# Kernel optimization log

Hardware: AMD Instinct MI355X
Metric: run time of the kernel (lower is better)

## Reference

```python
import jax, jax.numpy as jnp
import numpy as np

CHAN = 24
INNER = 64
GROUPS = 8
M = 5
LAM = 1e-4
MAX_ITER = 25
BETA = 1.0
EPS = 1e-5
B, HH, WW = 128, 32, 32


def conv2d(x, w, b=None):
    # NCHW, OIHW, 3x3 SAME conv (padding = kernel//2)
    y = jax.lax.conv_general_dilated(x, w, (1, 1), 'SAME',
                                     dimension_numbers=('NCHW', 'OIHW', 'NCHW'))
    if b is not None:
        y = y + b[None, :, None, None]
    return y


def group_norm(x, g, b):
    bsz, c, h, w = x.shape
    xg = x.reshape(bsz, GROUPS, c // GROUPS, h, w)
    mu = xg.mean(axis=(2, 3, 4), keepdims=True)
    var = xg.var(axis=(2, 3, 4), keepdims=True)
    xn = ((xg - mu) / jnp.sqrt(var + EPS)).reshape(bsz, c, h, w)
    return xn * g[None, :, None, None] + b[None, :, None, None]


def batch_norm(x, g, b):
    # training-mode batch statistics over (N, H, W)
    mu = x.mean(axis=(0, 2, 3), keepdims=True)
    var = x.var(axis=(0, 2, 3), keepdims=True)
    return (x - mu) / jnp.sqrt(var + EPS) * g[None, :, None, None] + b[None, :, None, None]


def resnet_f(p, z, x):
    c1w, g1g, g1b, c2w, g2g, g2b, g3g, g3b = p
    y = group_norm(jax.nn.relu(conv2d(z, c1w)), g1g, g1b)
    return group_norm(jax.nn.relu(z + group_norm(x + conv2d(y, c2w), g2g, g2b)), g3g, g3b)


def anderson(f, x0):
    # Anderson acceleration, fixed MAX_ITER iterations (no host-sync tol break).
    bsz = x0.shape[0]
    d = x0.size // bsz
    X = jnp.zeros((bsz, M, d), x0.dtype)
    Fm = jnp.zeros((bsz, M, d), x0.dtype)
    f0 = f(x0).reshape(bsz, -1)
    X = X.at[:, 0].set(x0.reshape(bsz, -1))
    Fm = Fm.at[:, 0].set(f0)
    X = X.at[:, 1].set(f0)
    Fm = Fm.at[:, 1].set(f(f0.reshape(x0.shape)).reshape(bsz, -1))
    for k in range(2, MAX_ITER):
        n = min(k, M)
        G = Fm[:, :n] - X[:, :n]                       # [b, n, d]
        Hm = jnp.zeros((bsz, n + 1, n + 1), x0.dtype)
        Hm = Hm.at[:, 0, 1:].set(1.0).at[:, 1:, 0].set(1.0)
        Hm = Hm.at[:, 1:, 1:].set(jnp.einsum('bnd,bmd->bnm', G, G)
                                  + LAM * jnp.eye(n, dtype=x0.dtype)[None])
        yv = jnp.zeros((bsz, n + 1, 1), x0.dtype).at[:, 0, 0].set(1.0)
        alpha = jnp.linalg.solve(Hm, yv)[:, 1:, 0]     # [b, n]
        xnew = (BETA * jnp.einsum('bn,bnd->bd', alpha, Fm[:, :n])
                + (1.0 - BETA) * jnp.einsum('bn,bnd->bd', alpha, X[:, :n]))
        X = X.at[:, k % M].set(xnew)
        Fm = Fm.at[:, k % M].set(f(xnew.reshape(x0.shape)).reshape(bsz, -1))
    return X[:, (MAX_ITER - 1) % M].reshape(x0.shape)


def setup_inputs() -> dict:
    key = jax.random.key(0)
    ks = jax.random.split(key, 8)
    inp = {
        'x': jax.random.normal(ks[0], (B, 3, HH, WW), jnp.float32),
        'pre_conv_w': jax.random.normal(ks[1], (CHAN, 3, 3, 3), jnp.float32) * 0.1,
        'pre_conv_b': jnp.zeros((CHAN,), jnp.float32),
        'pre_bn_g': jnp.ones((CHAN,), jnp.float32),
        'pre_bn_b': jnp.zeros((CHAN,), jnp.float32),
        'f_conv1_w': jax.random.normal(ks[2], (INNER, CHAN, 3, 3), jnp.float32) * 0.01,
        'gn1_g': jnp.ones((INNER,), jnp.float32),
        'gn1_b': jnp.zeros((INNER,), jnp.float32),
        'f_conv2_w': jax.random.normal(ks[3], (CHAN, INNER, 3, 3), jnp.float32) * 0.01,
        'gn2_g': jnp.ones((CHAN,), jnp.float32),
        'gn2_b': jnp.zeros((CHAN,), jnp.float32),
        'gn3_g': jnp.ones((CHAN,), jnp.float32),
        'gn3_b': jnp.zeros((CHAN,), jnp.float32),
        'post_bn_g': jnp.ones((CHAN,), jnp.float32),
        'post_bn_b': jnp.zeros((CHAN,), jnp.float32),
        'fc_w': jax.random.normal(ks[4], (10, CHAN * 4 * 4), jnp.float32) * 0.05,
        'fc_b': jnp.zeros((10,), jnp.float32),
    }
    return inp


def reference(x, pre_conv_w, pre_conv_b, pre_bn_g, pre_bn_b,
              f_conv1_w, gn1_g, gn1_b, f_conv2_w, gn2_g, gn2_b, gn3_g, gn3_b,
              post_bn_g, post_bn_b, fc_w, fc_b):
    # pre: conv + BatchNorm
    xp = batch_norm(conv2d(x, pre_conv_w, pre_conv_b), pre_bn_g, pre_bn_b)
    p = (f_conv1_w, gn1_g, gn1_b, f_conv2_w, gn2_g, gn2_b, gn3_g, gn3_b)
    # DEQ fixed-point solve (eval path: train=False returns the fixed point)
    z_star = anderson(lambda z: resnet_f(p, z, xp), jnp.zeros_like(xp))
    z = resnet_f(p, z_star, xp)
    # post: relu -> BN -> avgpool(8,8) -> flatten -> linear
    h = batch_norm(jax.nn.relu(z), post_bn_g, post_bn_b)
    bsz, c, hh, ww = h.shape
    pooled = h.reshape(bsz, c, hh // 8, 8, ww // 8, 8).mean(axis=(3, 5))  # [B,C,4,4]
    return pooled.reshape(bsz, -1) @ fc_w.T + fc_b
```

## Files before the change

### kernel.cpp

```cpp
#include <hip/hip_runtime.h>
#include <hip/hip_bf16.h>

typedef __hip_bfloat16 bf16;
typedef unsigned short ushortT;
typedef __attribute__((ext_vector_type(8))) short short8;
typedef __attribute__((ext_vector_type(4))) float f32x4;

#define BB 128
#define CHAN 24
#define INNER 64
#define HW 1024
#define DD (CHAN*HW)

constexpr size_t cBD = (size_t)BB*DD;
constexpr size_t cYB = (size_t)BB*INNER*HW;

__device__ __attribute__((aligned(16))) ushortT g_xp[cBD];
__device__ __attribute__((aligned(16))) ushortT g_X[5*cBD];
__device__ __attribute__((aligned(16))) ushortT g_F[5*cBD];
__device__ __attribute__((aligned(16))) ushortT g_G[5*cBD];
__device__ __attribute__((aligned(16))) ushortT g_yb[cYB];
__device__ __attribute__((aligned(16))) ushortT g_tb[cBD];
__device__ __attribute__((aligned(16))) ushortT g_w1m[9*64*32];
__device__ __attribute__((aligned(16))) ushortT g_w2m[9*24*64];
__device__ __attribute__((aligned(16))) float g_stats2a[48];
__device__ __attribute__((aligned(16))) float g_stats2b[48];
__device__ __attribute__((aligned(16))) float g_gn1sum[BB*8*2];
__device__ __attribute__((aligned(16))) float g_gn2sum[BB*24*2];
__device__ __attribute__((aligned(16))) float g_gram[BB*25];
__device__ __attribute__((aligned(16))) float g_params[5120];
__device__ unsigned g_isbf16;

#define P_PCW 0
#define P_PCB 648
#define P_PBG 672
#define P_PBB 696
#define P_G1G 720
#define P_G1B 784
#define P_G2G 848
#define P_G2B 872
#define P_G3G 896
#define P_G3B 920
#define P_POG 944
#define P_POB 968
#define P_FCW 992
#define P_FCB 4832

__device__ __forceinline__ size_t aidx(int b, int icv, int pix){
  return (((size_t)b*3 + icv)*1024 + (size_t)pix)*8;
}
__device__ __forceinline__ float rdin(const void* p, int i){
  if (g_isbf16) return __bfloat162float(((const bf16*)p)[i]);
  return ((const float*)p)[i];
}
__device__ __forceinline__ float b2f(ushortT u){
  unsigned v = ((unsigned)u) << 16;
  return __builtin_bit_cast(float, v);
}
__device__ __forceinline__ ushortT f2b(float f){
  unsigned u = __builtin_bit_cast(unsigned, f);
  u += 0x7FFFu + ((u >> 16) & 1u);
  return (ushortT)(u >> 16);
// ... 17 lines not shown
}

__global__ void detect_k(const void* g1g){
  if (threadIdx.x==0 && blockIdx.x==0){
    unsigned u = *(const unsigned*)g1g;
    g_isbf16 = (u == 0x3F803F80u) ? 1u : 0u;
  }
}

__global__ void cvt_params_k(const void* pcw, const void* pcb, const void* pbg, const void* pbb,
                             const void* g1g, const void* g1b, const void* g2g, const void* g2b,
                             const void* g3g, const void* g3b, const void* pog, const void* pob,
                             const void* fcw, const void* fcb){
  int t = threadIdx.x;
  for (int i=t;i<648;i+=256)  g_params[P_PCW+i]=rdin(pcw,i);
  for (int i=t;i<24;i+=256) { g_params[P_PCB+i]=rdin(pcb,i);
                              g_params[P_PBG+i]=rdin(pbg,i);
                              g_params[P_PBB+i]=rdin(pbb,i);
                              g_params[P_G2G+i]=rdin(g2g,i);
                              g_params[P_G2B+i]=rdin(g2b,i);
                              g_params[P_G3G+i]=rdin(g3g,i);
                              g_params[P_G3B+i]=rdin(g3b,i);
                              g_params[P_POG+i]=rdin(pog,i);
                              g_params[P_POB+i]=rdin(pob,i); }
  for (int i=t;i<64;i+=256) { g_params[P_G1G+i]=rdin(g1g,i);
                              g_params[P_G1B+i]=rdin(g1b,i); }
  for (int i=t;i<3840;i+=256) g_params[P_FCW+i]=rdin(fcw,i);
  for (int i=t;i<10;i+=256)   g_params[P_FCB+i]=rdin(fcb,i);
  for (int i=t;i<48;i+=256) { g_stats2a[i]=0.f; g_stats2b[i]=0.f; }
}

__global__ void wtm_k(const void* w1, const void* w2){
  int t = blockIdx.x*256 + threadIdx.x;
  if (t < 9*64*32){
    int ic = t & 31, oc = (t>>5)&63, s9 = t>>11;
    float v = (ic<24) ? rdin(w1, (oc*24+ic)*9 + s9) : 0.f;
    g_w1m[t] = f2b(v);
  }
  int u = t - 9*64*32;
  if (u >= 0 && u < 9*24*64){
    int ic = u & 63; int rest = u >> 6; int oc = rest % 24; int s9 = rest / 24;
    g_w2m[u] = f2b(rdin(w2, (oc*64+ic)*9 + s9));
  }
}

__global__ void zero0_k(){
  size_t base = ((size_t)blockIdx.x*256 + threadIdx.x)*8;
  short8 z = {0,0,0,0,0,0,0,0};
  *(short8*)&g_yb[base] = z;
  if (blockIdx.x < 1536) *(short8*)&g_X[base] = z;
  int t = blockIdx.x*256 + threadIdx.x;
  if (blockIdx.x < 8)  g_gn1sum[t] = 0.f;
  if (blockIdx.x < 24) g_gn2sum[t] = 0.f;
}

__global__ void preconv_k(const void* __restrict__ x){
  __shared__ float sR2d[4*48];
  int id = blockIdx.x*256 + threadIdx.x;
  int b = id >> 10, pix = id & 1023;
  int yy = pix >> 5, xx = pix & 31;
  float acc[24];
  #pragma unroll
  for (int oc=0;oc<24;oc++) acc[oc] = g_params[P_PCB+oc];
  for (int ic=0; ic<3; ic++)
    for (int ky=0; ky<3; ky++){
      int gy = yy+ky-1; if (gy<0||gy>=32) continue;
      for (int kx=0;kx<3;kx++){
        int gx = xx+kx-1; if (gx<0||gx>=32) continue;
        float v = rdin(x, ((b*3+ic)*32+gy)*32+gx);
        #pragma unroll
        for (int oc=0;oc<24;oc++)
          acc[oc] += v * g_params[P_PCW+(oc*3+ic)*9+ky*3+kx];
      }
    }
  st24c(g_tb, b, pix, acc);
  int lane = threadIdx.x & 63, wv = threadIdx.x >> 6;
  #pragma unroll
  for (int c=0;c<24;c++){
    float r = acc[c], q = acc[c]*acc[c];
    #pragma unroll
    for (int off=32;off;off>>=1){ r += __shfl_down(r,off,64); q += __shfl_down(q,off,64); }
    if (lane==0){ sR2d[wv*48+c*2]=r; sR2d[wv*48+c*2+1]=q; }
  }
  __syncthreads();
  if (threadIdx.x < 48)
    atomicAdd(&g_stats2a[threadIdx.x],
      sR2d[threadIdx.x] + sR2d[48+threadIdx.x] + sR2d[96+threadIdx.x] + sR2d[144+threadIdx.x]);
}

__global__ void bn_apply_k(){
  int id = blockIdx.x*256+threadIdx.x;
  int b = id >> 10, pix = id & 1023;
  const float inv = 1.f/(BB*HW);
  float tv[24], ov[24];
  ld24c(g_tb, b, pix, tv);
  #pragma unroll
  for (int c=0;c<24;c++){
    float mean = g_stats2a[c*2]*inv;
    float var = fmaxf(g_stats2a[c*2+1]*inv - mean*mean, 0.f);
    float rstd = rsqrtf(var + 1e-5f);
    ov[c] = (tv[c]-mean)*rstd*g_params[P_PBG+c] + g_params[P_PBB+c];
  }
  st24c(g_xp, b, pix, ov);
}

__launch_bounds__(256, 2)
__global__ void conv1_k(int s){
  __shared__ ushortT sMem[29312];
  ushortT* sA = sMem;
  ushortT* sW = sMem + 10880;
  const int tid = threadIdx.x;
  const int lane = tid & 63, wv = tid >> 6;
  const int mLane = lane & 15, q = lane >> 4;
  const int b = blockIdx.x >> 2, yt = blockIdx.x & 3;
  const ushortT* __restrict__ Xs = g_X + (size_t)s*cBD;
  if (blockIdx.x < 24) g_gn2sum[blockIdx.x*256 + tid] = 0.f;
  for (int i = tid; i < 1360; i += 256){
    int icv = i & 3, apix = i >> 2;
    int yl = apix / 34, xl = apix - yl*34;
    int gy = yt*8 - 1 + yl, gx = xl - 1;
    short8 v = {0,0,0,0,0,0,0,0};
    if (gy >= 0 && gy < 32 && gx >= 0 && gx < 32 && icv < 3)
      v = *(const short8*)&Xs[aidx(b, icv, gy*32 + gx)];
    *(short8*)&sA[(size_t)(apix*4 + (icv ^ (apix&3)))*8] = v;
  }
  for (int i = tid; i < 2304; i += 256){
    int icv = i & 3, rest = i >> 2;
    int oc = rest & 63, s9 = rest >> 6;
    short8 v = *(const short8*)&g_w1m[(size_t)((s9*64 + oc)*32) + icv*8];
    *(short8*)&sW[(size_t)((s9*64+oc)*4 + (icv ^ (oc&3)))*8] = v;
  }
  __syncthreads();
  f32x4 acc[4][4];
  #pragma unroll
  for (int mt=0;mt<4;mt++)
    #pragma unroll
    for (int nt=0;nt<4;nt++) acc[mt][nt] = (f32x4){0.f,0.f,0.f,0.f};
  for (int s9=0; s9<9; s9++){
    int ky = s9/3, kx = s9 - ky*3;
    short8 bfr[4];
    #pragma unroll
    for (int nt=0;nt<4;nt++){
      int oc = nt*16 + mLane;
      bfr[nt] = *(const short8*)&sW[(size_t)((s9*64+oc)*4 + (q ^ (oc&3)))*8];
    }
    #pragma unroll
    for (int mt=0;mt<4;mt++){
      int g = wv*4+mt;
      int apix = ((g>>1) + ky)*34 + (g&1)*16 + mLane + kx;
      short8 afr = *(const short8*)&sA[(size_t)(apix*4 + (q ^ (apix&3)))*8];
      #pragma unroll
      for (int nt=0;nt<4;nt++)
        acc[mt][nt] = __builtin_amdgcn_mfma_f32_16x16x32_bf16(afr, bfr[nt], acc[mt][nt], 0,0,0);
    }
  }
  __syncthreads();
  ushortT* sOut = sMem;
  #pragma unroll
  for (int mt=0;mt<4;mt++){
    int g = wv*4+mt;
    #pragma unroll
    for (int nt=0;nt<4;nt++){
      int oc = nt*16 + mLane;
      #pragma unroll
      for (int r=0;r<4;r++){
        int pix = (g>>1)*32 + (g&1)*16 + q*4 + r;
        sOut[pix*64 + oc] = f2b(fmaxf(acc[mt][nt][r], 0.f));
      }
    }
  }
  __syncthreads();
  float s0=0.f, s1=0.f;
  size_t gbase = ((size_t)b*1024 + yt*256)*64;
  for (int c = tid; c < 2048; c += 256){
    short8 v = *(const short8*)&sOut[c*8];
    *(short8*)&g_yb[gbase + (size_t)c*8] = v;
    #pragma unroll
    for (int j=0;j<8;j++){ float f = b2f((ushortT)v[j]); s0 += f; s1 += f*f; }
  }
  s0 += __shfl_down(s0,32); s1 += __shfl_down(s1,32);
  s0 += __shfl_down(s0,16); s1 += __shfl_down(s1,16);
  s0 += __shfl_down(s0, 8); s1 += __shfl_down(s1, 8);
  if (lane < 8){
    atomicAdd(&g_gn1sum[(b*8+lane)*2],   s0);
    atomicAdd(&g_gn1sum[(b*8+lane)*2+1], s1);
  }
}

__launch_bounds__(256, 2)
__global__ void conv2_k(){
  __shared__ ushortT sMem[35584];
  __shared__ float sAff[128];
  ushortT* sA = sMem;
  ushortT* sW = sMem + 21760;
  const int tid = threadIdx.x;
  const int lane = tid & 63, wv = tid >> 6;
  const int mLane = lane & 15, q = lane >> 4;
  const int b = blockIdx.x >> 2, yt = blockIdx.x & 3;
  if (tid < 64){
    int c = tid, gr = c>>3;
    float S = g_gn1sum[(b*8+gr)*2], Q = g_gn1sum[(b*8+gr)*2+1];
    float mean = S*(1.f/8192.f);
    float var = fmaxf(Q*(1.f/8192.f) - mean*mean, 0.f);
    float rstd = rsqrtf(var + 1e-5f);
    float sc = rstd*g_params[P_G1G+c];
    sAff[c] = sc; sAff[64+c] = g_params[P_G1B+c] - mean*sc;
  }
  __syncthreads();
  for (int i = tid; i < 2720; i += 256){
    int icv = i & 7, apix = i >> 3;
    int yl = apix / 34, xl = apix - yl*34;
    int gy = yt*8 - 1 + yl, gx = xl - 1;
    short8 v = {0,0,0,0,0,0,0,0};
    if (gy >= 0 && gy < 32 && gx >= 0 && gx < 32){
      short8 raw = *(const short8*)&g_yb[((size_t)b*1024 + gy*32+gx)*64 + icv*8];
      #pragma unroll
      for (int j=0;j<8;j++){
        int c = icv*8+j;
        v[j] = (short)f2b(b2f((ushortT)raw[j])*sAff[c] + sAff[64+c]);
      }
    }
    *(short8*)&sA[(size_t)(apix*8 + (icv ^ (apix&7)))*8] = v;
  }
  for (int i = tid; i < 1728; i += 256){
    int icv = i & 7, rest = i >> 3;
    int oc = rest % 24, s9 = rest / 24;
    short8 v = *(const short8*)&g_w2m[(size_t)((s9*24+oc)*64) + icv*8];
    *(short8*)&sW[(size_t)((s9*24+oc)*8 + (icv ^ (oc&7)))*8] = v;
  }
  __syncthreads();
  f32x4 acc[4][2];
  #pragma unroll
  for (int mt=0;mt<4;mt++){ acc[mt][0]=(f32x4){0.f,0.f,0.f,0.f}; acc[mt][1]=(f32x4){0.f,0.f,0.f,0.f}; }
  const bool nt1ok = (mLane < 8);
  for (int s9=0; s9<9; s9++){
    int ky = s9/3, kx = s9 - ky*3;
    #pragma unroll
    for (int ks=0; ks<2; ks++){
      int ib = ks*4;
      short8 bfr[2];
      { int oc = mLane;
        bfr[0] = *(const short8*)&sW[(size_t)((s9*24+oc)*8 + ((ib+q) ^ (oc&7)))*8]; }
      if (nt1ok){
        int oc = 16 + mLane;
        bfr[1] = *(const short8*)&sW[(size_t)((s9*24+oc)*8 + ((ib+q) ^ (oc&7)))*8];
      } else bfr[1] = (short8){0,0,0,0,0,0,0,0};
      #pragma unroll
      for (int mt=0;mt<4;mt++){
        int g = wv*4+mt;
        int apix = ((g>>1) + ky)*34 + (g&1)*16 + mLane + kx;
        short8 afr = *(const short8*)&sA[(size_t)(apix*8 + ((ib+q) ^ (apix&7)))*8];
        acc[mt][0] = __builtin_amdgcn_mfma_f32_16x16x32_bf16(afr, bfr[0], acc[mt][0], 0,0,0);
        acc[mt][1] = __builtin_amdgcn_mfma_f32_16x16x32_bf16(afr, bfr[1], acc[mt][1], 0,0,0);
      }
    }
  }
  #pragma unroll
  for (int nt=0;nt<2;nt++){
    int oc = nt*16 + mLane;
    bool ok = (oc < 24);
    int icv = oc >> 3, e = oc & 7;
    float s0=0.f, s1=0.f;
    if (ok){
      #pragma unroll
      for (int mt=0;mt<4;mt++){
        int g = wv*4+mt;
        #pragma unroll
        for (int r=0;r<4;r++){
          int pix = (yt*8 + (g>>1))*32 + (g&1)*16 + q*4 + r;
          size_t o = aidx(b, icv, pix) + e;
          float v = acc[mt][nt][r] + b2f(g_xp[o]);
          g_tb[o] = f2b(v);
          s0 += v; s1 += v*v;
        }
      }
    }
    s0 += __shfl_down(s0,32); s1 += __shfl_down(s1,32);
    s0 += __shfl_down(s0,16); s1 += __shfl_down(s1,16);
    if (lane < 16 && ok){
      atomicAdd(&g_gn2sum[(b*24+oc)*2],   s0);
      atomicAdd(&g_gn2sum[(b*24+oc)*2+1], s1);
    }
  }
}

template<int N>
__device__ __forceinline__ void chol_alpha(const float Kf[5][5], float* alpha){
  double K[N][N];
  #pragma unroll
  for (int i=0;i<N;i++)
    #pragma unroll
    for (int j=0;j<N;j++)
      K[i][j] = (double)Kf[i][j] + (i==j ? 1e-4 : 0.0);
  #pragma unroll
  for (int c=0;c<N;c++){
    double d = K[c][c];
    #pragma unroll
    for (int k2=0;k2<c;k2++) d -= K[c][k2]*K[c][k2];
    d = sqrt(fmax(d, 1e-300));
    K[c][c] = d;
    double inv = 1.0/d;
    #pragma unroll
    for (int r=c+1;r<N;r++){
      double v = K[r][c];
      #pragma unroll
      for (int k2=0;k2<c;k2++) v -= K[r][k2]*K[c][k2];
      K[r][c] = v*inv;
    }
  }
  double y[N];
  #pragma unroll
  for (int i=0;i<N;i++){
    double v = 1.0;
    #pragma unroll
    for (int j=0;j<i;j++) v -= K[i][j]*y[j];
    y[i] = v / K[i][i];
  }
  double w[N];
  #pragma unroll
  for (int i=N-1;i>=0;i--){
    double v = y[i];
    #pragma unroll
    for (int j=i+1;j<N;j++) v -= K[j][i]*w[j];
    w[i] = v / K[i][i];
  }
  double sum = 0.0;
  #pragma unroll
  for (int i=0;i<N;i++) sum += w[i];
  double invs = 1.0/sum;
  #pragma unroll
  for (int i=0;i<N;i++) alpha[i] = (float)(w[i]*invs);
}

__launch_bounds__(1024)
__global__ void fuse_k(int s, int n, int snext){
  __shared__ float sM2[8], sR2[8], sM3[8], sR3[8];
  __shared__ float sSc2[24], sSb2[24], sSc3[24], sSb3[24];
  __shared__ float sRed[16*16];
  __shared__ float sRedG[16*5];
  __shared__ float sAlpha[5];
  __shared__ float sStat[16*48];
  const int b = blockIdx.x;
  const int t = threadIdx.x;
  const int lane = t & 63, wv = t >> 6;
  if (t < 16) g_gn1sum[b*16 + t] = 0.f;
  if (t < 8){
    float S = g_gn2sum[(b*24+t*3)*2]   + g_gn2sum[(b*24+t*3+1)*2]   + g_gn2sum[(b*24+t*3+2)*2];
    float Q = g_gn2sum[(b*24+t*3)*2+1] + g_gn2sum[(b*24+t*3+1)*2+1] + g_gn2sum[(b*24+t*3+2)*2+1];
    float m = S*(1.f/3072.f);
    sM2[t] = m;
    sR2[t] = rsqrtf(fmaxf(Q*(1.f/3072.f) - m*m, 0.f) + 1e-5f);
  }
  __syncthreads();
  if (t < 24){
    int g = t/3;
    float sc = sR2[g]*g_params[P_G2G+t];
    sSc2[t] = sc; sSb2[t] = g_params[P_G2B+t] - sM2[g]*sc;
  }
  __syncthreads();
  float xv[24], v[24];
  ld24c(g_tb, b, t, v);
  ld24c(g_X + (size_t)s*cBD, b, t, xv);
  float p0[8], p1[8];
  #pragma unroll
  for (int g=0;g<8;g++){ p0[g]=0.f; p1[g]=0.f; }
  #pragma unroll
  for (int c=0;c<24;c++){
    float val = fmaxf(xv[c] + v[c]*sSc2[c] + sSb2[c], 0.f);
    v[c] = val;
    int g = c/3;
    p0[g] += val; p1[g] += val*val;
  }
  #pragma unroll
  for (int g=0;g<8;g++){
    #pragma unroll
    for (int off=32;off;off>>=1){ p0[g]+=__shfl_down(p0[g],off,64); p1[g]+=__shfl_down(p1[g],off,64); }
  }
  if (lane==0){
    #pragma unroll
    for (int g=0;g<8;g++){ sRed[wv*16+g*2]=p0[g]; sRed[wv*16+g*2+1]=p1[g]; }
  }
  __syncthreads();
  if (t < 8){
    float S=0.f, Q=0.f;
    #pragma unroll
    for (int w=0;w<16;w++){ S += sRed[w*16+t*2]; Q += sRed[w*16+t*2+1]; }
    float m = S*(1.f/3072.f);
    sM3[t] = m;
    sR3[t] = rsqrtf(fmaxf(Q*(1.f/3072.f) - m*m, 0.f) + 1e-5f);
  }
  __syncthreads();
  if (t < 24){
    int g = t/3;
    float sc = sR3[g]*g_params[P_G3G+t];
    sSc3[t] = sc; sSb3[t] = g_params[P_G3B+t] - sM3[g]*sc;
  }
  __syncthreads();
  float fv[24];
  #pragma unroll
  for (int c=0;c<24;c++) fv[c] = v[c]*sSc3[c] + sSb3[c];
  st24c(g_F + (size_t)s*cBD, b, t, fv);

  if (n > 0){
    float gl[24];
    #pragma unroll
    for (int c=0;c<24;c++) gl[c] = b2f(f2b(fv[c] - xv[c]));
    st24c(g_G + (size_t)s*cBD, b, t, gl);
    float part[5];
    #pragma unroll
    for (int j=0;j<5;j++) part[j] = 0.f;
    #pragma unroll
    for (int j=0;j<5;j++){
      if (j >= n) continue;
      float acc = 0.f;
      if (j == s){
        #pragma unroll
        for (int c=0;c<24;c++) acc += gl[c]*gl[c];
      } else {
        float gv[24];
        ld24c(g_G + (size_t)j*cBD, b, t, gv);
        #pragma unroll
        for (int c=0;c<24;c++) acc += gl[c]*gv[c];
      }
      part[j] = acc;
    }
    #pragma unroll
    for (int j=0;j<5;j++){
      float vv = part[j];
      #pragma unroll
      for (int off=32;off;off>>=1) vv += __shfl_down(vv,off,64);
      if (lane==0) sRedG[wv*5+j] = vv;
    }
    __syncthreads();
    if (t == 0){
      for (int j=0;j<n;j++){
        float vv = 0.f;
        for (int w=0;w<16;w++) vv += sRedG[w*5+j];
        g_gram[b*25+s*5+j] = vv;
        g_gram[b*25+j*5+s] = vv;
      }
      float Kf[5][5];
      for (int i=0;i<n;i++)
        for (int j=0;j<n;j++) Kf[i][j] = g_gram[b*25+i*5+j];
      float al[5];
      if (n==1) al[0]=1.f;
      else if (n==2) chol_alpha<2>(Kf, al);
      else if (n==3) chol_alpha<3>(Kf, al);
      else if (n==4) chol_alpha<4>(Kf, al);
      else chol_alpha<5>(Kf, al);
      for (int j=0;j<n;j++) sAlpha[j] = al[j];
    }
    __syncthreads();
    float acc[24];
    #pragma unroll
    for (int c=0;c<24;c++) acc[c] = 0.f;
    #pragma unroll
    for (int j=0;j<5;j++){
      if (j >= n) continue;
      float aj = sAlpha[j];
      if (j == s){
        #pragma unroll
        for (int c=0;c<24;c++) acc[c] += aj*b2f(f2b(fv[c]));
      } else {
        float tv2[24];
        ld24c(g_F + (size_t)j*cBD, b, t, tv2);
        #pragma unroll
        for (int c=0;c<24;c++) acc[c] += aj*tv2[c];
      }
    }
    st24c(g_X + (size_t)snext*cBD, b, t, acc);
  } else {
    #pragma unroll
    for (int c=0;c<24;c++){
      float r = fmaxf(b2f(f2b(fv[c])), 0.f);
      float q = r*r;
      #pragma unroll
      for (int off=32;off;off>>=1){ r += __shfl_down(r,off,64); q += __shfl_down(q,off,64); }
      if (lane==0){ sStat[wv*48+c*2]=r; sStat[wv*48+c*2+1]=q; }
    }
    __syncthreads();
    if (t < 48){
      float vv = 0.f;
      #pragma unroll
      for (int w=0;w<16;w++) vv += sStat[w*48+t];
      atomicAdd(&g_stats2b[t], vv);
    }
  }
}

__global__ void postfc_k(void* __restrict__ out){
  __shared__ float sPool[384];
  __shared__ float sMean[24], sRstd[24];
  int b = blockIdx.x, t = threadIdx.x;
  if (t < 24){
    const float inv = 1.f/(BB*HW);
    float mean = g_stats2b[t*2]*inv;
    float var = fmaxf(g_stats2b[t*2+1]*inv - mean*mean, 0.f);
    sMean[t] = mean; sRstd[t] = rsqrtf(var + 1e-5f);
  }
  __syncthreads();
  const ushortT* z = g_F + 4*cBD;
  for (int i=t; i<384; i+=256){
    int c = i>>4, bin = i&15, ph = bin>>2, pw = bin&3;
    int icv = c>>3, e = c&7;
    float gg = g_params[P_POG+c], bv = g_params[P_POB+c];
    float mean = sMean[c], rstd = sRstd[c];
    float sum = 0.f;
    for (int dy=0;dy<8;dy++)
      for (int dx=0;dx<8;dx++){
        int pix = (ph*8+dy)*32 + pw*8+dx;
        float vv = fmaxf(b2f(z[aidx(b,icv,pix) + e]), 0.f);
        sum += (vv-mean)*rstd*gg + bv;
      }
    sPool[i] = sum*(1.f/64.f);
  }
  __syncthreads();
  if (t < 10){
    float s2 = g_params[P_FCB+t];
    for (int k2=0;k2<384;k2++) s2 += sPool[k2]*g_params[P_FCW+t*384+k2];
    if (g_isbf16) ((bf16*)out)[b*10+t] = __float2bfloat16(s2);
    else ((float*)out)[b*10+t] = s2;
  }
}

extern "C" void kernel_launch(void* const* d_in, const int* in_sizes, int n_in,
                              void* d_out, int out_size, void* d_ws, size_t ws_size,
                              hipStream_t stream){
  const void* x   = d_in[0];
  const void* pcw = d_in[1];
  const void* pcb = d_in[2];
  const void* pbg = d_in[3];
  const void* pbb = d_in[4];
  const void* w1  = d_in[5];
  const void* g1g = d_in[6];
  const void* g1b = d_in[7];
  const void* w2  = d_in[8];
  const void* g2g = d_in[9];
  const void* g2b = d_in[10];
  const void* g3g = d_in[11];
  const void* g3b = d_in[12];
  const void* pog = d_in[13];
  const void* pob = d_in[14];
  const void* fcw = d_in[15];
  const void* fcb = d_in[16];
  (void)d_ws; (void)ws_size; (void)in_sizes; (void)n_in; (void)out_size;

  detect_k<<<1,64,0,stream>>>(g1g);
  cvt_params_k<<<1,256,0,stream>>>(pcw,pcb,pbg,pbb,g1g,g1b,g2g,g2b,g3g,g3b,pog,pob,fcw,fcb);
  wtm_k<<<126,256,0,stream>>>(w1, w2);

  preconv_k<<<512,256,0,stream>>>(x);
  bn_apply_k<<<512,256,0,stream>>>();

  zero0_k<<<4096,256,0,stream>>>();
  conv2_k<<<512,256,0,stream>>>();
  fuse_k<<<128,1024,0,stream>>>(0, 1, 1);

  for (int k=1;k<25;k++){
    int s = k%5;
    conv1_k<<<512,256,0,stream>>>(s);
    conv2_k<<<512,256,0,stream>>>();
    if (k < 24){
      int n = (k+1 < 5) ? (k+1) : 5;
      fuse_k<<<128,1024,0,stream>>>(s, n, (k+1)%5);
    } else {
      fuse_k<<<128,1024,0,stream>>>(s, 0, -1);
    }
  }

  postfc_k<<<128,256,0,stream>>>(d_out);
}
```

Baseline: 1.452 ms.

## Fuse entire Anderson DEQ loop into one persistent per-sample megakernel

Replaces the 75 per-iteration conv1/conv2/fuse launches with a single 128-block, 1024-thread kernel. Each block owns one sample and keeps the iterate, the conv1 activations and the weights in LDS across all 25 iterations. Group-norm statistics and the Gram matrix move from global atomics to LDS, and the activation layout changes to channel-major. This removes launch overhead and the global round trips of intermediates, but runs only 128 blocks with very large LDS per block, which limits occupancy.

```diff
diff --git a/kernel.cpp b/kernel.cpp
--- a/kernel.cpp
+++ b/kernel.cpp
@@ -4,6 +4,7 @@
 typedef __hip_bfloat16 bf16;
 typedef unsigned short ushortT;
 typedef __attribute__((ext_vector_type(8))) short short8;
+typedef __attribute__((ext_vector_type(4))) short s16x4;
 typedef __attribute__((ext_vector_type(4))) float f32x4;
 
 #define BB 128
@@ -13,21 +14,16 @@
 #define DD (CHAN*HW)
 
 constexpr size_t cBD = (size_t)BB*DD;
-constexpr size_t cYB = (size_t)BB*INNER*HW;
 
 __device__ __attribute__((aligned(16))) ushortT g_xp[cBD];
-__device__ __attribute__((aligned(16))) ushortT g_X[5*cBD];
+__device__ __attribute__((aligned(16))) ushortT g_tb[cBD];
+__device__ __attribute__((aligned(16))) ushortT g_xcur[cBD];
 __device__ __attribute__((aligned(16))) ushortT g_F[5*cBD];
 __device__ __attribute__((aligned(16))) ushortT g_G[5*cBD];
-__device__ __attribute__((aligned(16))) ushortT g_yb[cYB];
-__device__ __attribute__((aligned(16))) ushortT g_tb[cBD];
-__device__ __attribute__((aligned(16))) ushortT g_w1m[9*64*32];
-__device__ __attribute__((aligned(16))) ushortT g_w2m[9*24*64];
+__device__ __attribute__((aligned(16))) ushortT g_w1m[9*4*64*8];
+__device__ __attribute__((aligned(16))) ushortT g_w2m[9*8*24*8];
 __device__ __attribute__((aligned(16))) float g_stats2a[48];
 __device__ __attribute__((aligned(16))) float g_stats2b[48];
-__device__ __attribute__((aligned(16))) float g_gn1sum[BB*8*2];
-__device__ __attribute__((aligned(16))) float g_gn2sum[BB*24*2];
-__device__ __attribute__((aligned(16))) float g_gram[BB*25];
 __device__ __attribute__((aligned(16))) float g_params[5120];
 __device__ unsigned g_isbf16;
 
@@ -111,26 +107,19 @@
 
 __global__ void wtm_k(const void* w1, const void* w2){
   int t = blockIdx.x*256 + threadIdx.x;
-  if (t < 9*64*32){
-    int ic = t & 31, oc = (t>>5)&63, s9 = t>>11;
+  if (t < 9*4*64*8){
+    int e = t & 7, oc = (t>>3)&63, chk = (t>>9)&3, s9 = t>>11;
+    int ic = chk*8 + e;
     float v = (ic<24) ? rdin(w1, (oc*24+ic)*9 + s9) : 0.f;
     g_w1m[t] = f2b(v);
   }
-  int u = t - 9*64*32;
-  if (u >= 0 && u < 9*24*64){
-    int ic = u & 63; int rest = u >> 6; int oc = rest % 24; int s9 = rest / 24;
+  int u = t - 9*4*64*8;
+  if (u >= 0 && u < 9*8*24*8){
+    int e = u & 7; int rest = u >> 3; int oc = rest % 24; rest /= 24;
+    int chk = rest & 7, s9 = rest >> 3;
+    int ic = chk*8 + e;
     g_w2m[u] = f2b(rdin(w2, (oc*64+ic)*9 + s9));
   }
-}
-
-__global__ void zero0_k(){
-  size_t base = ((size_t)blockIdx.x*256 + threadIdx.x)*8;
-  short8 z = {0,0,0,0,0,0,0,0};
-  *(short8*)&g_yb[base] = z;
-  if (blockIdx.x < 1536) *(short8*)&g_X[base] = z;
-  int t = blockIdx.x*256 + threadIdx.x;
-  if (blockIdx.x < 8)  g_gn1sum[t] = 0.f;
-  if (blockIdx.x < 24) g_gn2sum[t] = 0.f;
 }
 
 __global__ void preconv_k(const void* __restrict__ x){
@@ -171,195 +160,15 @@
   int id = blockIdx.x*256+threadIdx.x;
   int b = id >> 10, pix = id & 1023;
   const float inv = 1.f/(BB*HW);
-  float tv[24], ov[24];
+  float tv[24];
   ld24c(g_tb, b, pix, tv);
   #pragma unroll
   for (int c=0;c<24;c++){
     float mean = g_stats2a[c*2]*inv;
     float var = fmaxf(g_stats2a[c*2+1]*inv - mean*mean, 0.f);
     float rstd = rsqrtf(var + 1e-5f);
-    ov[c] = (tv[c]-mean)*rstd*g_params[P_PBG+c] + g_params[P_PBB+c];
-  }
-  st24c(g_xp, b, pix, ov);
-}
-
-__launch_bounds__(256, 2)
-__global__ void conv1_k(int s){
-  __shared__ ushortT sMem[29312];
-  ushortT* sA = sMem;
-  ushortT* sW = sMem + 10880;
-  const int tid = threadIdx.x;
-  const int lane = tid & 63, wv = tid >> 6;
-  const int mLane = lane & 15, q = lane >> 4;
-  const int b = blockIdx.x >> 2, yt = blockIdx.x & 3;
-  const ushortT* __restrict__ Xs = g_X + (size_t)s*cBD;
-  if (blockIdx.x < 24) g_gn2sum[blockIdx.x*256 + tid] = 0.f;
-  for (int i = tid; i < 1360; i += 256){
-    int icv = i & 3, apix = i >> 2;
-    int yl = apix / 34, xl = apix - yl*34;
-    int gy = yt*8 - 1 + yl, gx = xl - 1;
-    short8 v = {0,0,0,0,0,0,0,0};
-    if (gy >= 0 && gy < 32 && gx >= 0 && gx < 32 && icv < 3)
-      v = *(const short8*)&Xs[aidx(b, icv, gy*32 + gx)];
-    *(short8*)&sA[(size_t)(apix*4 + (icv ^ (apix&3)))*8] = v;
-  }
-  for (int i = tid; i < 2304; i += 256){
-    int icv = i & 3, rest = i >> 2;
-    int oc = rest & 63, s9 = rest >> 6;
-    short8 v = *(const short8*)&g_w1m[(size_t)((s9*64 + oc)*32) + icv*8];
-    *(short8*)&sW[(size_t)((s9*64+oc)*4 + (icv ^ (oc&3)))*8] = v;
-  }
-  __syncthreads();
-  f32x4 acc[4][4];
-  #pragma unroll
-  for (int mt=0;mt<4;mt++)
-    #pragma unroll
-    for (int nt=0;nt<4;nt++) acc[mt][nt] = (f32x4){0.f,0.f,0.f,0.f};
-  for (int s9=0; s9<9; s9++){
-    int ky = s9/3, kx = s9 - ky*3;
-    short8 bfr[4];
-    #pragma unroll
-    for (int nt=0;nt<4;nt++){
-      int oc = nt*16 + mLane;
-      bfr[nt] = *(const short8*)&sW[(size_t)((s9*64+oc)*4 + (q ^ (oc&3)))*8];
-    }
-    #pragma unroll
-    for (int mt=0;mt<4;mt++){
-      int g = wv*4+mt;
-      int apix = ((g>>1) + ky)*34 + (g&1)*16 + mLane + kx;
-      short8 afr = *(const short8*)&sA[(size_t)(apix*4 + (q ^ (apix&3)))*8];
-      #pragma unroll
-      for (int nt=0;nt<4;nt++)
-        acc[mt][nt] = __builtin_amdgcn_mfma_f32_16x16x32_bf16(afr, bfr[nt], acc[mt][nt], 0,0,0);
-    }
-  }
-  __syncthreads();
-  ushortT* sOut = sMem;
-  #pragma unroll
-  for (int mt=0;mt<4;mt++){
-    int g = wv*4+mt;
-    #pragma unroll
-    for (int nt=0;nt<4;nt++){
-      int oc = nt*16 + mLane;
-      #pragma unroll
-      for (int r=0;r<4;r++){
-        int pix = (g>>1)*32 + (g&1)*16 + q*4 + r;
-        sOut[pix*64 + oc] = f2b(fmaxf(acc[mt][nt][r], 0.f));
-      }
-    }
-  }
-  __syncthreads();
-  float s0=0.f, s1=0.f;
-  size_t gbase = ((size_t)b*1024 + yt*256)*64;
-  for (int c = tid; c < 2048; c += 256){
-    short8 v = *(const short8*)&sOut[c*8];
-    *(short8*)&g_yb[gbase + (size_t)c*8] = v;
-    #pragma unroll
-    for (int j=0;j<8;j++){ float f = b2f((ushortT)v[j]); s0 += f; s1 += f*f; }
-  }
-  s0 += __shfl_down(s0,32); s1 += __shfl_down(s1,32);
-  s0 += __shfl_down(s0,16); s1 += __shfl_down(s1,16);
-  s0 += __shfl_down(s0, 8); s1 += __shfl_down(s1, 8);
-  if (lane < 8){
-    atomicAdd(&g_gn1sum[(b*8+lane)*2],   s0);
-    atomicAdd(&g_gn1sum[(b*8+lane)*2+1], s1);
-  }
-}
-
-__launch_bounds__(256, 2)
-__global__ void conv2_k(){
-  __shared__ ushortT sMem[35584];
-  __shared__ float sAff[128];
-  ushortT* sA = sMem;
-  ushortT* sW = sMem + 21760;
-  const int tid = threadIdx.x;
-  const int lane = tid & 63, wv = tid >> 6;
-  const int mLane = lane & 15, q = lane >> 4;
-  const int b = blockIdx.x >> 2, yt = blockIdx.x & 3;
-  if (tid < 64){
-    int c = tid, gr = c>>3;
-    float S = g_gn1sum[(b*8+gr)*2], Q = g_gn1sum[(b*8+gr)*2+1];
-    float mean = S*(1.f/8192.f);
-    float var = fmaxf(Q*(1.f/8192.f) - mean*mean, 0.f);
-    float rstd = rsqrtf(var + 1e-5f);
-    float sc = rstd*g_params[P_G1G+c];
-    sAff[c] = sc; sAff[64+c] = g_params[P_G1B+c] - mean*sc;
-  }
-  __syncthreads();
-  for (int i = tid; i < 2720; i += 256){
-    int icv = i & 7, apix = i >> 3;
-    int yl = apix / 34, xl = apix - yl*34;
-    int gy = yt*8 - 1 + yl, gx = xl - 1;
-    short8 v = {0,0,0,0,0,0,0,0};
-    if (gy >= 0 && gy < 32 && gx >= 0 && gx < 32){
-      short8 raw = *(const short8*)&g_yb[((size_t)b*1024 + gy*32+gx)*64 + icv*8];
-      #pragma unroll
-      for (int j=0;j<8;j++){
-        int c = icv*8+j;
-        v[j] = (short)f2b(b2f((ushortT)raw[j])*sAff[c] + sAff[64+c]);
-      }
-    }
-    *(short8*)&sA[(size_t)(apix*8 + (icv ^ (apix&7)))*8] = v;
-  }
-  for (int i = tid; i < 1728; i += 256){
-    int icv = i & 7, rest = i >> 3;
-    int oc = rest % 24, s9 = rest / 24;
-    short8 v = *(const short8*)&g_w2m[(size_t)((s9*24+oc)*64) + icv*8];
-    *(short8*)&sW[(size_t)((s9*24+oc)*8 + (icv ^ (oc&7)))*8] = v;
-  }
-  __syncthreads();
-  f32x4 acc[4][2];
-  #pragma unroll
-  for (int mt=0;mt<4;mt++){ acc[mt][0]=(f32x4){0.f,0.f,0.f,0.f}; acc[mt][1]=(f32x4){0.f,0.f,0.f,0.f}; }
-  const bool nt1ok = (mLane < 8);
-  for (int s9=0; s9<9; s9++){
-    int ky = s9/3, kx = s9 - ky*3;
-    #pragma unroll
-    for (int ks=0; ks<2; ks++){
-      int ib = ks*4;
-      short8 bfr[2];
-      { int oc = mLane;
-        bfr[0] = *(const short8*)&sW[(size_t)((s9*24+oc)*8 + ((ib+q) ^ (oc&7)))*8]; }
-      if (nt1ok){
-        int oc = 16 + mLane;
-        bfr[1] = *(const short8*)&sW[(size_t)((s9*24+oc)*8 + ((ib+q) ^ (oc&7)))*8];
-      } else bfr[1] = (short8){0,0,0,0,0,0,0,0};
-      #pragma unroll
-      for (int mt=0;mt<4;mt++){
-        int g = wv*4+mt;
-        int apix = ((g>>1) + ky)*34 + (g&1)*16 + mLane + kx;
-        short8 afr = *(const short8*)&sA[(size_t)(apix*8 + ((ib+q) ^ (apix&7)))*8];
-        acc[mt][0] = __builtin_amdgcn_mfma_f32_16x16x32_bf16(afr, bfr[0], acc[mt][0], 0,0,0);
-        acc[mt][1] = __builtin_amdgcn_mfma_f32_16x16x32_bf16(afr, bfr[1], acc[mt][1], 0,0,0);
-      }
-    }
-  }
-  #pragma unroll
-  for (int nt=0;nt<2;nt++){
-    int oc = nt*16 + mLane;
-    bool ok = (oc < 24);
-    int icv = oc >> 3, e = oc & 7;
-    float s0=0.f, s1=0.f;
-    if (ok){
-      #pragma unroll
-      for (int mt=0;mt<4;mt++){
-        int g = wv*4+mt;
-        #pragma unroll
-        for (int r=0;r<4;r++){
-          int pix = (yt*8 + (g>>1))*32 + (g&1)*16 + q*4 + r;
-          size_t o = aidx(b, icv, pix) + e;
-          float v = acc[mt][nt][r] + b2f(g_xp[o]);
-          g_tb[o] = f2b(v);
-          s0 += v; s1 += v*v;
-        }
-      }
-    }
-    s0 += __shfl_down(s0,32); s1 += __shfl_down(s1,32);
-    s0 += __shfl_down(s0,16); s1 += __shfl_down(s1,16);
-    if (lane < 16 && ok){
-      atomicAdd(&g_gn2sum[(b*24+oc)*2],   s0);
-      atomicAdd(&g_gn2sum[(b*24+oc)*2+1], s1);
-    }
+    float ov = (tv[c]-mean)*rstd*g_params[P_PBG+c] + g_params[P_PBB+c];
+    g_xp[((size_t)b*24+c)*1024 + pix] = f2b(ov);
   }
 }
 
@@ -411,158 +220,364 @@
   for (int i=0;i<N;i++) alpha[i] = (float)(w[i]*invs);
 }
 
+#define MEGA_SMEM 161024
+
 __launch_bounds__(1024)
-__global__ void fuse_k(int s, int n, int snext){
-  __shared__ float sM2[8], sR2[8], sM3[8], sR3[8];
-  __shared__ float sSc2[24], sSb2[24], sSc3[24], sSb3[24];
-  __shared__ float sRed[16*16];
-  __shared__ float sRedG[16*5];
-  __shared__ float sAlpha[5];
-  __shared__ float sStat[16*48];
+__global__ void mega_k(){
+  extern __shared__ __align__(16) ushortT sU[];
+  ushortT* sX  = sU;
+  ushortT* sW1 = sU + 24576;
+  ushortT* sYb = sU;
+  ushortT* sW2 = sU + 65536;
+  float* sS = (float*)(sU + 79360);
+  float* sStat1 = sS;
+  float* sAff1  = sS + 128;
+  float* sStat2 = sS + 256;
+  float* sAff2  = sS + 304;
+  float* sStat3 = sS + 352;
+  float* sAff3  = sS + 368;
+  float* sGram  = sS + 416;
+  float* sAlpha = sS + 441;
+  float* sRedG  = sS + 448;
+  float* sPost  = sS + 528;
+
   const int b = blockIdx.x;
   const int t = threadIdx.x;
   const int lane = t & 63, wv = t >> 6;
-  if (t < 16) g_gn1sum[b*16 + t] = 0.f;
-  if (t < 8){
-    float S = g_gn2sum[(b*24+t*3)*2]   + g_gn2sum[(b*24+t*3+1)*2]   + g_gn2sum[(b*24+t*3+2)*2];
-    float Q = g_gn2sum[(b*24+t*3)*2+1] + g_gn2sum[(b*24+t*3+1)*2+1] + g_gn2sum[(b*24+t*3+2)*2+1];
-    float m = S*(1.f/3072.f);
-    sM2[t] = m;
-    sR2[t] = rsqrtf(fmaxf(Q*(1.f/3072.f) - m*m, 0.f) + 1e-5f);
-  }
-  __syncthreads();
-  if (t < 24){
-    int g = t/3;
-    float sc = sR2[g]*g_params[P_G2G+t];
-    sSc2[t] = sc; sSb2[t] = g_params[P_G2B+t] - sM2[g]*sc;
-  }
-  __syncthreads();
-  float xv[24], v[24];
-  ld24c(g_tb, b, t, v);
-  ld24c(g_X + (size_t)s*cBD, b, t, xv);
-  float p0[8], p1[8];
-  #pragma unroll
-  for (int g=0;g<8;g++){ p0[g]=0.f; p1[g]=0.f; }
-  #pragma unroll
-  for (int c=0;c<24;c++){
-    float val = fmaxf(xv[c] + v[c]*sSc2[c] + sSb2[c], 0.f);
-    v[c] = val;
-    int g = c/3;
-    p0[g] += val; p1[g] += val*val;
-  }
-  #pragma unroll
-  for (int g=0;g<8;g++){
-    #pragma unroll
-    for (int off=32;off;off>>=1){ p0[g]+=__shfl_down(p0[g],off,64); p1[g]+=__shfl_down(p1[g],off,64); }
-  }
-  if (lane==0){
-    #pragma unroll
-    for (int g=0;g<8;g++){ sRed[wv*16+g*2]=p0[g]; sRed[wv*16+g*2+1]=p1[g]; }
-  }
-  __syncthreads();
-  if (t < 8){
-    float S=0.f, Q=0.f;
-    #pragma unroll
-    for (int w=0;w<16;w++){ S += sRed[w*16+t*2]; Q += sRed[w*16+t*2+1]; }
-    float m = S*(1.f/3072.f);
-    sM3[t] = m;
-    sR3[t] = rsqrtf(fmaxf(Q*(1.f/3072.f) - m*m, 0.f) + 1e-5f);
-  }
-  __syncthreads();
-  if (t < 24){
-    int g = t/3;
-    float sc = sR3[g]*g_params[P_G3G+t];
-    sSc3[t] = sc; sSb3[t] = g_params[P_G3B+t] - sM3[g]*sc;
-  }
-  __syncthreads();
-  float fv[24];
-  #pragma unroll
-  for (int c=0;c<24;c++) fv[c] = v[c]*sSc3[c] + sSb3[c];
-  st24c(g_F + (size_t)s*cBD, b, t, fv);
-
-  if (n > 0){
-    float gl[24];
-    #pragma unroll
-    for (int c=0;c<24;c++) gl[c] = b2f(f2b(fv[c] - xv[c]));
-    st24c(g_G + (size_t)s*cBD, b, t, gl);
-    float part[5];
-    #pragma unroll
-    for (int j=0;j<5;j++) part[j] = 0.f;
-    #pragma unroll
-    for (int j=0;j<5;j++){
-      if (j >= n) continue;
-      float acc = 0.f;
-      if (j == s){
-        #pragma unroll
-        for (int c=0;c<24;c++) acc += gl[c]*gl[c];
-      } else {
-        float gv[24];
-        ld24c(g_G + (size_t)j*cBD, b, t, gv);
-        #pragma unroll
-        for (int c=0;c<24;c++) acc += gl[c]*gv[c];
-      }
-      part[j] = acc;
-    }
-    #pragma unroll
-    for (int j=0;j<5;j++){
-      float vv = part[j];
-      #pragma unroll
-      for (int off=32;off;off>>=1) vv += __shfl_down(vv,off,64);
-      if (lane==0) sRedG[wv*5+j] = vv;
-    }
-    __syncthreads();
-    if (t == 0){
-      for (int j=0;j<n;j++){
-        float vv = 0.f;
-        for (int w=0;w<16;w++) vv += sRedG[w*5+j];
-        g_gram[b*25+s*5+j] = vv;
-        g_gram[b*25+j*5+s] = vv;
-      }
-      float Kf[5][5];
-      for (int i=0;i<n;i++)
-        for (int j=0;j<n;j++) Kf[i][j] = g_gram[b*25+i*5+j];
+  const int mLane = lane & 15, q = lane >> 4;
+  const int g0 = wv*4;
+  const bool ntOK = (mLane < 8);
+  const size_t xpb = (size_t)b*DD;
+
+  for (int i=t; i<1728; i+=1024)
+    *(short8*)&sW2[(size_t)i*8] = *(const short8*)&g_w2m[(size_t)i*8];
+  {
+    short8 z = {0,0,0,0,0,0,0,0};
+    for (int i=t; i<3072; i+=1024) *(short8*)&sX[(size_t)i*8] = z;
+    for (int i=t; i<3072; i+=1024) *(short8*)&g_xcur[xpb + (size_t)i*8] = z;
+  }
+
+  #pragma unroll 1
+  for (int k=0; k<25; ++k){
+    const int s = k % 5;
+    const bool fin = (k == 24);
+    const int n = fin ? 0 : ((k+1 < 5) ? (k+1) : 5);
+
+    for (int i=t; i<2304; i+=1024)
+      *(short8*)&sW1[(size_t)i*8] = *(const short8*)&g_w1m[(size_t)i*8];
+    if (t < 128) sStat1[t] = 0.f;
+    else if (t < 176) sStat2[t-128] = 0.f;
+    else if (t < 192) sStat3[t-176] = 0.f;
+    else if (t < 240) sPost[t-192] = 0.f;
+    __syncthreads();
+
+    f32x4 a1[4][4];
+    #pragma unroll
+    for (int mt=0;mt<4;mt++)
+      #pragma unroll
+      for (int nt=0;nt<4;nt++) a1[mt][nt] = (f32x4){0.f,0.f,0.f,0.f};
+    for (int s9=0; s9<9; ++s9){
+      const int ky = s9/3, kx = s9 - ky*3;
+      short8 bfr[4];
+      #pragma unroll
+      for (int nt=0;nt<4;nt++)
+        bfr[nt] = *(const short8*)&sW1[(size_t)(((s9*4+q)*64) + nt*16 + mLane)*8];
+      #pragma unroll
+      for (int mt=0;mt<4;mt++){
+        const int g = g0+mt;
+        const int gy = (g>>1) + ky - 1;
+        const int gx = (g&1)*16 + mLane + kx - 1;
+        short8 afr = {0,0,0,0,0,0,0,0};
+        if (q < 3 && gy >= 0 && gy < 32 && gx >= 0 && gx < 32)
+          afr = *(const short8*)&sX[(size_t)(q*1024 + gy*32 + gx)*8];
+        #pragma unroll
+        for (int nt=0;nt<4;nt++)
+          a1[mt][nt] = __builtin_amdgcn_mfma_f32_16x16x32_bf16(afr, bfr[nt], a1[mt][nt], 0,0,0);
+      }
+    }
+    #pragma unroll
+    for (int nt=0;nt<4;nt++){
+      float s0=0.f, s1=0.f;
+      #pragma unroll
+      for (int mt=0;mt<4;mt++)
+        #pragma unroll
+        for (int r=0;r<4;r++){
+          float v = b2f(f2b(fmaxf(a1[mt][nt][r], 0.f)));
+          a1[mt][nt][r] = v;
+          s0 += v; s1 += v*v;
+        }
+      s0 += __shfl_xor(s0,16,64); s1 += __shfl_xor(s1,16,64);
+      s0 += __shfl_xor(s0,32,64); s1 += __shfl_xor(s1,32,64);
+      if (q == 0){
+        atomicAdd(&sStat1[(nt*16+mLane)*2],   s0);
+        atomicAdd(&sStat1[(nt*16+mLane)*2+1], s1);
+      }
+    }
+    __syncthreads();
+    if (t < 64){
+      const int c = t, gr = c>>3;
+      float S=0.f, Q=0.f;
+      #pragma unroll
+      for (int j2=0;j2<8;j2++){ S += sStat1[(gr*8+j2)*2]; Q += sStat1[(gr*8+j2)*2+1]; }
+      float mean = S*(1.f/8192.f);
+      float var  = fmaxf(Q*(1.f/8192.f) - mean*mean, 0.f);
+      float rstd = rsqrtf(var + 1e-5f);
+      float sc = rstd*g_params[P_G1G+c];
+      sAff1[c] = sc; sAff1[64+c] = g_params[P_G1B+c] - mean*sc;
+    }
+    __syncthreads();
+    #pragma unroll
+    for (int nt=0;nt<4;nt++){
+      const int oc = nt*16 + mLane;
+      const float sc = sAff1[oc], sb = sAff1[64+oc];
+      const size_t cb = (size_t)(oc>>3)*8192 + (oc&7);
+      #pragma unroll
+      for (int mt=0;mt<4;mt++){
+        const int pb = (g0+mt)*16 + q*4;
+        #pragma unroll
+        for (int r=0;r<4;r++)
+          sYb[cb + (size_t)(pb+r)*8] = f2b(a1[mt][nt][r]*sc + sb);
+      }
+    }
+    __syncthreads();
+
+    f32x4 a2[4][2];
+    #pragma unroll
+    for (int mt=0;mt<4;mt++){ a2[mt][0]=(f32x4){0.f,0.f,0.f,0.f}; a2[mt][1]=(f32x4){0.f,0.f,0.f,0.f}; }
+    for (int s9=0; s9<9; ++s9){
+      const int ky = s9/3, kx = s9 - ky*3;
+      #pragma unroll
+      for (int ks=0; ks<2; ++ks){
+        const int ch = ks*4 + q;
+        short8 b0 = *(const short8*)&sW2[(size_t)(((s9*8+ch)*24) + mLane)*8];
+        short8 b1 = ntOK ? *(const short8*)&sW2[(size_t)(((s9*8+ch)*24) + 16 + mLane)*8]
+                         : (short8){0,0,0,0,0,0,0,0};
+        #pragma unroll
+        for (int mt=0;mt<4;mt++){
+          const int g = g0+mt;
+          const int gy = (g>>1) + ky - 1;
+          const int gx = (g&1)*16 + mLane + kx - 1;
+          short8 afr = {0,0,0,0,0,0,0,0};
+          if (gy>=0 && gy<32 && gx>=0 && gx<32)
+            afr = *(const short8*)&sYb[(size_t)(ch*1024 + gy*32 + gx)*8];
+          a2[mt][0] = __builtin_amdgcn_mfma_f32_16x16x32_bf16(afr, b0, a2[mt][0], 0,0,0);
+          a2[mt][1] = __builtin_amdgcn_mfma_f32_16x16x32_bf16(afr, b1, a2[mt][1], 0,0,0);
+        }
+      }
+    }
+
+    #pragma unroll
+    for (int ci=0; ci<2; ++ci){
+      const int c = ci*16 + mLane;
+      const bool ok = (ci==0) || ntOK;
+      float s0=0.f, s1=0.f;
+      if (ok){
+        #pragma unroll
+        for (int mt=0;mt<4;mt++){
+          const int p0 = (g0+mt)*16 + q*4;
+          s16x4 xpv = *(const s16x4*)&g_xp[xpb + (size_t)c*1024 + p0];
+          #pragma unroll
+          for (int r=0;r<4;r++){
+            float v = a2[mt][ci][r] + b2f((ushortT)xpv[r]);
+            a2[mt][ci][r] = v;
+            s0 += v; s1 += v*v;
+          }
+        }
+      }
+      s0 += __shfl_xor(s0,16,64); s1 += __shfl_xor(s1,16,64);
+      s0 += __shfl_xor(s0,32,64); s1 += __shfl_xor(s1,32,64);
+      if (q==0 && ok){
+        atomicAdd(&sStat2[c*2],   s0);
+        atomicAdd(&sStat2[c*2+1], s1);
+      }
+    }
+    __syncthreads();
+    if (t < 24){
+      const int gr = t/3;
+      float S = sStat2[(gr*3)*2]+sStat2[(gr*3+1)*2]+sStat2[(gr*3+2)*2];
+      float Q = sStat2[(gr*3)*2+1]+sStat2[(gr*3+1)*2+1]+sStat2[(gr*3+2)*2+1];
+      float m = S*(1.f/3072.f);
+      float rstd = rsqrtf(fmaxf(Q*(1.f/3072.f)-m*m,0.f)+1e-5f);
+      float sc = rstd*g_params[P_G2G+t];
+      sAff2[t] = sc; sAff2[24+t] = g_params[P_G2B+t] - m*sc;
+    }
+    __syncthreads();
+    s16x4 xvp[2][4];
+    #pragma unroll
+    for (int ci=0; ci<2; ++ci){
+      const int c = ci*16 + mLane;
+      const bool ok = (ci==0) || ntOK;
+      float s0=0.f, s1=0.f;
+      if (ok){
+        const float sc = sAff2[c], sb = sAff2[24+c];
+        #pragma unroll
+        for (int mt=0;mt<4;mt++){
+          const int p0 = (g0+mt)*16 + q*4;
+          xvp[ci][mt] = *(const s16x4*)&g_xcur[xpb + (size_t)c*1024 + p0];
+          #pragma unroll
+          for (int r=0;r<4;r++){
+            float tv = b2f(f2b(a2[mt][ci][r]));
+            float val = fmaxf(b2f((ushortT)xvp[ci][mt][r]) + tv*sc + sb, 0.f);
+            a2[mt][ci][r] = val;
+            s0 += val; s1 += val*val;
+          }
+        }
+      }
+      s0 += __shfl_xor(s0,16,64); s1 += __shfl_xor(s1,16,64);
+      s0 += __shfl_xor(s0,32,64); s1 += __shfl_xor(s1,32,64);
+      if (q==0 && ok){
+        atomicAdd(&sStat3[(c/3)*2],   s0);
+        atomicAdd(&sStat3[(c/3)*2+1], s1);
+      }
+    }
+    __syncthreads();
+    if (t < 24){
+      const int gr = t/3;
+      float m = sStat3[gr*2]*(1.f/3072.f);
+      float rstd = rsqrtf(fmaxf(sStat3[gr*2+1]*(1.f/3072.f)-m*m,0.f)+1e-5f);
+      float sc = rstd*g_params[P_G3G+t];
+      sAff3[t] = sc; sAff3[24+t] = g_params[P_G3B+t] - m*sc;
+    }
+    __syncthreads();
+    const size_t fb = (size_t)s*cBD + xpb;
+    s16x4 fvp[2][4], glp[2][4];
+    #pragma unroll
+    for (int ci=0; ci<2; ++ci){
+      const int c = ci*16 + mLane;
+      const bool ok = (ci==0) || ntOK;
+      if (ok){
+        const float sc = sAff3[c], sb = sAff3[24+c];
+        #pragma unroll
+        for (int mt=0;mt<4;mt++){
+          const int p0 = (g0+mt)*16 + q*4;
+          s16x4 fo, go;
+          #pragma unroll
+          for (int r=0;r<4;r++){
+            float fv = a2[mt][ci][r]*sc + sb;
+            fo[r] = (short)f2b(fv);
+            go[r] = (short)f2b(fv - b2f((ushortT)xvp[ci][mt][r]));
+          }
+          fvp[ci][mt] = fo; glp[ci][mt] = go;
+          *(s16x4*)&g_F[fb + (size_t)c*1024 + p0] = fo;
+          if (!fin) *(s16x4*)&g_G[fb + (size_t)c*1024 + p0] = go;
+        }
+      }
+    }
+    if (!fin){
+      float part[5];
+      #pragma unroll
+      for (int j=0;j<5;j++) part[j]=0.f;
+      #pragma unroll
+      for (int j=0;j<5;j++){
+        if (j < n){
+          float acc=0.f;
+          #pragma unroll
+          for (int ci=0; ci<2; ++ci){
+            const int c = ci*16 + mLane;
+            const bool ok = (ci==0) || ntOK;
+            if (!ok) continue;
+            #pragma unroll
+            for (int mt=0;mt<4;mt++){
+              if (j == s){
+                #pragma unroll
+                for (int r=0;r<4;r++){ float g2 = b2f((ushortT)glp[ci][mt][r]); acc += g2*g2; }
+              } else {
+                const int p0 = (g0+mt)*16 + q*4;
+                s16x4 gj = *(const s16x4*)&g_G[(size_t)j*cBD + xpb + (size_t)c*1024 + p0];
+                #pragma unroll
+                for (int r=0;r<4;r++) acc += b2f((ushortT)glp[ci][mt][r])*b2f((ushortT)gj[r]);
+              }
+            }
+          }
+          part[j] = acc;
+        }
+      }
+      #pragma unroll
+      for (int j=0;j<5;j++){
+        float v = part[j];
+        v += __shfl_xor(v,1,64);  v += __shfl_xor(v,2,64);
+        v += __shfl_xor(v,4,64);  v += __shfl_xor(v,8,64);
+        v += __shfl_xor(v,16,64); v += __shfl_xor(v,32,64);
+        if (lane==0) sRedG[wv*5+j] = v;
+      }
+      __syncthreads();
+      if (t == 0){
+        for (int j=0;j<n;j++){
+          float v = 0.f;
+          for (int w=0;w<16;w++) v += sRedG[w*5+j];
+          sGram[s*5+j] = v; sGram[j*5+s] = v;
+        }
+        float Kf[5][5];
+        for (int i=0;i<n;i++)
+          for (int j=0;j<n;j++) Kf[i][j] = sGram[i*5+j];
+        float al[5];
+        if (n==1) al[0]=1.f;
+        else if (n==2) chol_alpha<2>(Kf, al);
+        else if (n==3) chol_alpha<3>(Kf, al);
+        else if (n==4) chol_alpha<4>(Kf, al);
+        else chol_alpha<5>(Kf, al);
+        for (int j=0;j<n;j++) sAlpha[j] = al[j];
+      }
+      __syncthreads();
       float al[5];
-      if (n==1) al[0]=1.f;
-      else if (n==2) chol_alpha<2>(Kf, al);
-      else if (n==3) chol_alpha<3>(Kf, al);
-      else if (n==4) chol_alpha<4>(Kf, al);
-      else chol_alpha<5>(Kf, al);
-      for (int j=0;j<n;j++) sAlpha[j] = al[j];
-    }
-    __syncthreads();
-    float acc[24];
-    #pragma unroll
-    for (int c=0;c<24;c++) acc[c] = 0.f;
-    #pragma unroll
-    for (int j=0;j<5;j++){
-      if (j >= n) continue;
-      float aj = sAlpha[j];
-      if (j == s){
-        #pragma unroll
-        for (int c=0;c<24;c++) acc[c] += aj*b2f(f2b(fv[c]));
-      } else {
-        float tv2[24];
-        ld24c(g_F + (size_t)j*cBD, b, t, tv2);
-        #pragma unroll
-        for (int c=0;c<24;c++) acc[c] += aj*tv2[c];
-      }
-    }
-    st24c(g_X + (size_t)snext*cBD, b, t, acc);
-  } else {
-    #pragma unroll
-    for (int c=0;c<24;c++){
-      float r = fmaxf(b2f(f2b(fv[c])), 0.f);
-      float q = r*r;
-      #pragma unroll
-      for (int off=32;off;off>>=1){ r += __shfl_down(r,off,64); q += __shfl_down(q,off,64); }
-      if (lane==0){ sStat[wv*48+c*2]=r; sStat[wv*48+c*2+1]=q; }
-    }
-    __syncthreads();
-    if (t < 48){
-      float vv = 0.f;
-      #pragma unroll
-      for (int w=0;w<16;w++) vv += sStat[w*48+t];
-      atomicAdd(&g_stats2b[t], vv);
+      #pragma unroll
+      for (int j=0;j<5;j++) al[j] = (j<n) ? sAlpha[j] : 0.f;
+      #pragma unroll
+      for (int ci=0; ci<2; ++ci){
+        const int c = ci*16 + mLane;
+        const bool ok = (ci==0) || ntOK;
+        if (!ok) continue;
+        const int chk = c>>3, e = c&7;
+        #pragma unroll
+        for (int mt=0;mt<4;mt++){
+          const int p0 = (g0+mt)*16 + q*4;
+          float xn[4] = {0.f,0.f,0.f,0.f};
+          #pragma unroll
+          for (int j=0;j<5;j++){
+            if (j < n){
+              if (j == s){
+                #pragma unroll
+                for (int r=0;r<4;r++) xn[r] += al[j]*b2f((ushortT)fvp[ci][mt][r]);
+              } else {
+                s16x4 fj = *(const s16x4*)&g_F[(size_t)j*cBD + xpb + (size_t)c*1024 + p0];
+                #pragma unroll
+                for (int r=0;r<4;r++) xn[r] += al[j]*b2f((ushortT)fj[r]);
+              }
+            }
+          }
+          s16x4 xo;
+          #pragma unroll
+          for (int r=0;r<4;r++) xo[r] = (short)f2b(xn[r]);
+          *(s16x4*)&g_xcur[xpb + (size_t)c*1024 + p0] = xo;
+          #pragma unroll
+          for (int r=0;r<4;r++)
+            sX[(size_t)(chk*1024 + p0 + r)*8 + e] = (ushortT)xo[r];
+        }
+      }
+    } else {
+      #pragma unroll
+      for (int ci=0; ci<2; ++ci){
+        const int c = ci*16 + mLane;
+        const bool ok = (ci==0) || ntOK;
+        float s0=0.f, s1=0.f;
+        if (ok){
+          #pragma unroll
+          for (int mt=0;mt<4;mt++)
+            #pragma unroll
+            for (int r=0;r<4;r++){
+              float v = fmaxf(b2f((ushortT)fvp[ci][mt][r]), 0.f);
+              s0 += v; s1 += v*v;
+            }
+        }
+        s0 += __shfl_xor(s0,16,64); s1 += __shfl_xor(s1,16,64);
+        s0 += __shfl_xor(s0,32,64); s1 += __shfl_xor(s1,32,64);
+        if (q==0 && ok){
+          atomicAdd(&sPost[c*2],   s0);
+          atomicAdd(&sPost[c*2+1], s1);
+        }
+      }
+      __syncthreads();
+      if (t < 48) atomicAdd(&g_stats2b[t], sPost[t]);
     }
   }
 }
@@ -578,17 +593,16 @@
     sMean[t] = mean; sRstd[t] = rsqrtf(var + 1e-5f);
   }
   __syncthreads();
-  const ushortT* z = g_F + 4*cBD;
+  const ushortT* z = g_F + 4*cBD + (size_t)b*DD;
   for (int i=t; i<384; i+=256){
     int c = i>>4, bin = i&15, ph = bin>>2, pw = bin&3;
-    int icv = c>>3, e = c&7;
     float gg = g_params[P_POG+c], bv = g_params[P_POB+c];
     float mean = sMean[c], rstd = sRstd[c];
     float sum = 0.f;
     for (int dy=0;dy<8;dy++)
       for (int dx=0;dx<8;dx++){
         int pix = (ph*8+dy)*32 + pw*8+dx;
-        float vv = fmaxf(b2f(z[aidx(b,icv,pix) + e]), 0.f);
+        float vv = fmaxf(b2f(z[(size_t)c*1024 + pix]), 0.f);
         sum += (vv-mean)*rstd*gg + bv;
       }
     sPool[i] = sum*(1.f/64.f);
@@ -624,6 +638,13 @@
   const void* fcb = d_in[16];
   (void)d_ws; (void)ws_size; (void)in_sizes; (void)n_in; (void)out_size;
 
+  static bool attrSet = false;
+  if (!attrSet){
+    hipFuncSetAttribute(reinterpret_cast<const void*>(mega_k),
+                        hipFuncAttributeMaxDynamicSharedMemorySize, MEGA_SMEM);
+    attrSet = true;
+  }
+
   detect_k<<<1,64,0,stream>>>(g1g);
   cvt_params_k<<<1,256,0,stream>>>(pcw,pcb,pbg,pbb,g1g,g1b,g2g,g2b,g3g,g3b,pog,pob,fcw,fcb);
   wtm_k<<<126,256,0,stream>>>(w1, w2);
@@ -631,21 +652,7 @@
   preconv_k<<<512,256,0,stream>>>(x);
   bn_apply_k<<<512,256,0,stream>>>();
 
-  zero0_k<<<4096,256,0,stream>>>();
-  conv2_k<<<512,256,0,stream>>>();
-  fuse_k<<<128,1024,0,stream>>>(0, 1, 1);
-
-  for (int k=1;k<25;k++){
-    int s = k%5;
-    conv1_k<<<512,256,0,stream>>>(s);
-    conv2_k<<<512,256,0,stream>>>();
-    if (k < 24){
-      int n = (k+1 < 5) ? (k+1) : 5;
-      fuse_k<<<128,1024,0,stream>>>(s, n, (k+1)%5);
-    } else {
-      fuse_k<<<128,1024,0,stream>>>(s, 0, -1);
-    }
-  }
+  mega_k<<<128,1024,MEGA_SMEM,stream>>>();
 
   postfc_k<<<128,256,0,stream>>>(d_out);
 }
```

Result: slower. 3.264 ms (+124.8%).
